# Kernel tuning notes

Hardware: AMD Instinct MI355X
Metric: run time of the kernel (lower is better)

## Reference

```python
import jax, jax.numpy as jnp
import numpy as np
from jax import lax

VOCAB, EMBED, HIDDEN, LAYERS = 32000, 256, 384, 6
B, S = 16, 512
SCALE = 0.05  # keep tanh out of saturation

def setup_inputs() -> dict:
    key = jax.random.key(0)
    ks = jax.random.split(key, 10)
    return {
        "x": jax.random.randint(ks[0], (B, S), 0, VOCAB),
        "emb": jax.random.normal(ks[1], (VOCAB, EMBED), jnp.float32) * SCALE,
        "W_ih0": jax.random.normal(ks[2], (HIDDEN, EMBED), jnp.float32) * SCALE,
        "W_ih": jax.random.normal(ks[3], (LAYERS - 1, HIDDEN, HIDDEN), jnp.float32) * SCALE,
        "W_hh": jax.random.normal(ks[4], (LAYERS, HIDDEN, HIDDEN), jnp.float32) * SCALE,
        "b_ih": jax.random.normal(ks[5], (LAYERS, HIDDEN), jnp.float32) * SCALE,
        "b_hh": jax.random.normal(ks[6], (LAYERS, HIDDEN), jnp.float32) * SCALE,
        "W_out": jax.random.normal(ks[7], (VOCAB, HIDDEN), jnp.float32) * SCALE,
        "b_out": jax.random.normal(ks[8], (VOCAB,), jnp.float32) * SCALE,
    }

def _rnn_layer(seq, Wi, Wh, bi, bh):
    # seq: [S, B, in_dim]; Elman: h_t = tanh(x_t Wi^T + bi + h_{t-1} Wh^T + bh)
    pre = jnp.einsum('sbi,hi->sbh', seq, Wi) + bi  # batched input projection
    h0 = jnp.zeros((seq.shape[1], Wh.shape[0]), seq.dtype)
    def step(h, p):
        h = jnp.tanh(p + h @ Wh.T + bh)
        return h, h
    _, out = lax.scan(step, h0, pre)
    return out  # [S, B, H]

def reference(x, emb, W_ih0, W_ih, W_hh, b_ih, b_hh, W_out, b_out):
    seq = jnp.swapaxes(emb[x], 0, 1)  # [S, B, E]
    for l in range(LAYERS):
        Wi = W_ih0 if l == 0 else W_ih[l - 1]
        seq = _rnn_layer(seq, Wi, W_hh[l], b_ih[l], b_hh[l])
        # inter-layer dropout: identity in eval mode
    out = jnp.swapaxes(seq, 0, 1)  # [B, S, H]
    return out @ W_out.T + b_out  # [B, S, V]
```

## Files before the change

kernel.cpp:

```cpp
#include <hip/hip_runtime.h>

typedef _Float16 f16;
typedef _Float16 f16x8 __attribute__((ext_vector_type(8)));
typedef _Float16 f16x4 __attribute__((ext_vector_type(4)));
typedef float f32x4 __attribute__((ext_vector_type(4)));

#define MFMA16(a, b, c) __builtin_amdgcn_mfma_f32_16x16x32_f16(a, b, c, 0, 0, 0)

#define CH 8
#define NCH 64
#define SLOT_F (CH * 24 * 64 * 4)

__device__ __forceinline__ float fast_tanh(float x) {
    float e = __builtin_amdgcn_exp2f(x * 2.885390081777927f);
    return 1.0f - 2.0f * __builtin_amdgcn_rcpf(e + 1.0f);
}

__device__ __forceinline__ void lds_barrier() {
    asm volatile("s_waitcnt lgkmcnt(0)" ::: "memory");
    __builtin_amdgcn_s_barrier();
    __builtin_amdgcn_sched_barrier(0);
}

__device__ __forceinline__ void wait_flag(const int* f, int target) {
    if (threadIdx.x == 0) {
        while (__hip_atomic_load(f, __ATOMIC_ACQUIRE, __HIP_MEMORY_SCOPE_AGENT) < target) {
            __builtin_amdgcn_s_sleep(1);
        }
    }
    __syncthreads();
}
__device__ __forceinline__ void set_flag(int* f, int val) {
    __syncthreads();
    if (threadIdx.x == 0)
        __hip_atomic_store(f, val, __ATOMIC_RELEASE, __HIP_MEMORY_SCOPE_AGENT);
}

__global__ void cvt_kernel(const float* __restrict__ src, f16* __restrict__ dst, const int n4) {
    const int i = blockIdx.x * blockDim.x + threadIdx.x;
    if (i < n4) {
        const float4 v = ((const float4*)src)[i];
        f16x4 o = { (f16)v.x, (f16)v.y, (f16)v.z, (f16)v.w };
        *(f16x4*)(dst + (size_t)i * 4) = o;
    }
}

__global__ void bias_combine_kernel(const float* __restrict__ b_ih, const float* __restrict__ b_hh,
                                    float* __restrict__ bias_c) {
    const int i = blockIdx.x * blockDim.x + threadIdx.x;
    if (i < 6 * 384) bias_c[i] = b_ih[i] + b_hh[i];
}

__global__ void embed_kernel(const int* __restrict__ x, const float* __restrict__ emb,
                             f16* __restrict__ seq0) {
    const int token = blockIdx.x;
    const int s = token >> 4, b = token & 15;
    const int idx = x[b * 512 + s];
    const float4 v = ((const float4*)(emb + (size_t)idx * 256))[threadIdx.x];
    f16x4 o = { (f16)v.x, (f16)v.y, (f16)v.z, (f16)v.w };
    *(f16x4*)(seq0 + (size_t)token * 256 + threadIdx.x * 4) = o;
}

template<int NK>
__device__ __forceinline__ void a_role(const f16* __restrict__ in_seq,
                                       const f16* __restrict__ Wi,
                                       const float* __restrict__ bias,
                                       float* __restrict__ preL,
                                       const int* flag_in, int* flag_pre, const int* flag_seq,
                                       const int L) {
    const int tid = threadIdx.x, lane = tid & 63, w = tid >> 6;
    const int lr = lane & 15, lq = lane >> 4;
    const int KIN = NK * 32;

    f16x8 WiF[6][NK];
#pragma unroll
    for (int i = 0; i < 6; ++i) {
        const f16* wrow = Wi + (size_t)((w * 6 + i) * 16 + lr) * KIN + lq * 8;
#pragma unroll
        for (int kk = 0; kk < NK; ++kk) WiF[i][kk] = *(const f16x8*)(wrow + kk * 32);
    }
    float bv[6];
#pragma unroll
    for (int i = 0; i < 6; ++i) bv[i] = bias[(w * 6 + i) * 16 + lr];

    for (int c = 0; c < NCH; ++c) {
        if (L > 0) wait_flag(flag_in, c + 1);
        if (c >= 4) wait_flag(flag_seq, c - 3);

        float* slot = preL + (size_t)(c & 3) * SLOT_F;
#pragma unroll
        for (int g = 0; g < 2; ++g) {
            f32x4 acc[4][6];
#pragma unroll
            for (int s = 0; s < 4; ++s)
#pragma unroll
                for (int i = 0; i < 6; ++i) acc[s][i] = (f32x4){ bv[i], bv[i], bv[i], bv[i] };

            const int t0 = c * CH + g * 4;
#pragma unroll
            for (int kk = 0; kk < NK; ++kk) {
                f16x8 a[4];
#pragma unroll
                for (int s = 0; s < 4; ++s)
                    a[s] = *(const f16x8*)(in_seq + (size_t)((t0 + s) * 16 + lr) * KIN + kk * 32 + lq * 8);
#pragma unroll
                for (int s = 0; s < 4; ++s)
#pragma unroll
                    for (int i = 0; i < 6; ++i) acc[s][i] = MFMA16(a[s], WiF[i][kk], acc[s][i]);
            }
#pragma unroll
            for (int s = 0; s < 4; ++s)
#pragma unroll
                for (int i = 0; i < 6; ++i)
                    *(f32x4*)(slot + ((size_t)((g * 4 + s) * 24 + w * 6 + i) * 64 + lane) * 4) = acc[s][i];
        }
        set_flag(flag_pre, c + 1);
    }
}

__device__ __forceinline__ void b_role(const float* __restrict__ preL,
                                       const f16* __restrict__ Wh,
                                       f16* __restrict__ out_seq,
                                       const int* flag_pre, int* flag_seq,
                                       f16 (*hbuf)[16][392]) {
    const int tid = threadIdx.x, lane = tid & 63, w = tid >> 6;
    const int lr = lane & 15, lq = lane >> 4, kb = lq * 8;

    for (int i = tid; i < 2 * 16 * 392; i += 256) (&hbuf[0][0][0])[i] = (f16)0.0f;

    f16x8 WhF[6][12];
#pragma unroll
    for (int i = 0; i < 6; ++i) {
        const f16* wrow = Wh + (size_t)((w * 6 + i) * 16 + lr) * 384 + kb;
#pragma unroll
        for (int kk = 0; kk < 12; ++kk) WhF[i][kk] = *(const f16x8*)(wrow + kk * 32);
    }
    __syncthreads();

    const int crow = tid >> 4;
    const int ccol = (tid & 15) * 8;

    for (int c = 0; c < NCH; ++c) {
        wait_flag(flag_pre, c + 1);
        const float* slot = preL + (size_t)(c & 3) * SLOT_F;

#pragma unroll
        for (int g = 0; g < 2; ++g) {
            f32x4 pre_[4][6];
#pragma unroll
            for (int s = 0; s < 4; ++s)
#pragma unroll
                for (int i = 0; i < 6; ++i)
                    pre_[s][i] = *(const f32x4*)(slot + ((size_t)((g * 4 + s) * 24 + w * 6 + i) * 64 + lane) * 4);

#pragma unroll
            for (int s4 = 0; s4 < 4; ++s4) {
                const int sc = g * 4 + s4;
                const int t = c * CH + sc;
                f32x4 acc[6];
#pragma unroll
                for (int i = 0; i < 6; ++i) acc[i] = (f32x4){ 0.f, 0.f, 0.f, 0.f };

                const f16* hb = &hbuf[sc & 1][0][0] + lr * 392 + kb;
#pragma unroll
                for (int kk = 0; kk < 12; ++kk) {
                    const f16x8 a = *(const f16x8*)(hb + kk * 32);
#pragma unroll
                    for (int i = 0; i < 6; ++i) acc[i] = MFMA16(a, WhF[i][kk], acc[i]);
                }

                f16* hn = &hbuf[(sc + 1) & 1][0][0];
#pragma unroll
                for (int i = 0; i < 6; ++i) {
                    const int n = (w * 6 + i) * 16 + lr;
#pragma unroll
                    for (int r = 0; r < 4; ++r) {
                        const float v = acc[i][r] + pre_[s4][i][r];
                        hn[(lq * 4 + r) * 392 + n] = (f16)fast_tanh(v);
                    }
                }
                lds_barrier();
                const f16* hs = &hbuf[(sc + 1) & 1][0][0] + crow * 392 + ccol;
                f16* og = out_seq + (size_t)(t * 16 + crow) * 384 + ccol;
#pragma unroll
                for (int p = 0; p < 3; ++p)
                    *(f16x8*)(og + p * 128) = *(const f16x8*)(hs + p * 128);
            }
        }
        set_flag(flag_seq, c + 1);
    }
}

__global__ __launch_bounds__(256, 1) void pipeline_kernel(
    const f16* __restrict__ seq0, const f16* __restrict__ Wi0,
    const f16* __restrict__ WiR, const f16* __restrict__ WhAll,
    const float* __restrict__ biasAll, f16* __restrict__ sA, f16* __restrict__ sB,
    float* __restrict__ preRing, int* __restrict__ flags) {
    __shared__ f16 hbuf[2][16][392];
    const int bid = blockIdx.x;
    if (bid < 6) {
        const int L = bid;
        const f16* in_seq = (L == 0) ? seq0 : ((L & 1) ? sA : sB);
        const f16* Wi = (L == 0) ? Wi0 : (WiR + (size_t)(L - 1) * 384 * 384);
        float* preL = preRing + (size_t)L * 4 * SLOT_F;
        if (L == 0)
            a_role<8>(in_seq, Wi, biasAll, preL, nullptr, flags + 8, flags + 0, 0);
        else
            a_role<12>(in_seq, Wi, biasAll + L * 384, preL, flags + (L - 1), flags + 8 + L, flags + L, L);
    } else {
        const int L = bid - 6;
        f16* outb = (L & 1) ? sB : sA;
        b_role(preRing + (size_t)L * 4 * SLOT_F, WhAll + (size_t)L * 384 * 384, outb,
               flags + 8 + L, flags + L, hbuf);
    }
}

__global__ __launch_bounds__(256) void out_proj_kernel(
    const f16* __restrict__ A, const f16* __restrict__ Bm,
    const float* __restrict__ bias, float* __restrict__ C) {
    __shared__ f16 As[128][40];
    __shared__ f16 Bs[128][40];
    const int tid = threadIdx.x, lane = tid & 63, w = tid >> 6;
    const int lr = lane & 15, lq = lane >> 4;
    const int bm = blockIdx.x, bn = blockIdx.y;
    const int wm = w >> 1, wn = w & 1;

    f32x4 acc[4][4];
#pragma unroll
    for (int i = 0; i < 4; ++i)
#pragma unroll
        for (int j = 0; j < 4; ++j) acc[i][j] = (f32x4){ 0.f, 0.f, 0.f, 0.f };

    const int sr = tid >> 1, sh = tid & 1;
    const f16* Ag = A + (size_t)(bm * 128 + sr) * 384 + sh * 16;
    const f16* Bg = Bm + (size_t)(bn * 128 + sr) * 384 + sh * 16;

    for (int kt = 0; kt < 12; ++kt) {
        const f16x8 a0 = *(const f16x8*)(Ag + kt * 32);
        const f16x8 a1 = *(const f16x8*)(Ag + kt * 32 + 8);
        const f16x8 b0 = *(const f16x8*)(Bg + kt * 32);
        const f16x8 b1 = *(const f16x8*)(Bg + kt * 32 + 8);
        *(f16x8*)(&As[sr][sh * 16]) = a0;
        *(f16x8*)(&As[sr][sh * 16 + 8]) = a1;
        *(f16x8*)(&Bs[sr][sh * 16]) = b0;
        *(f16x8*)(&Bs[sr][sh * 16 + 8]) = b1;
        __syncthreads();
        f16x8 af[4], bf[4];
#pragma unroll
        for (int mi = 0; mi < 4; ++mi) af[mi] = *(const f16x8*)(&As[wm * 64 + mi * 16 + lr][lq * 8]);
#pragma unroll
        for (int ni = 0; ni < 4; ++ni) bf[ni] = *(const f16x8*)(&Bs[wn * 64 + ni * 16 + lr][lq * 8]);
#pragma unroll
        for (int mi = 0; mi < 4; ++mi)
#pragma unroll
            for (int ni = 0; ni < 4; ++ni) acc[mi][ni] = MFMA16(af[mi], bf[ni], acc[mi][ni]);
        __syncthreads();
    }

    float bv[4];
#pragma unroll
    for (int ni = 0; ni < 4; ++ni) bv[ni] = bias[bn * 128 + wn * 64 + ni * 16 + lr];
#pragma unroll
    for (int mi = 0; mi < 4; ++mi) {
#pragma unroll
        for (int rr = 0; rr < 4; ++rr) {
            const int m = bm * 128 + wm * 64 + mi * 16 + lq * 4 + rr;
            const int s = m >> 4, b = m & 15;
            float* crow = C + (size_t)(b * 512 + s) * 32000;
#pragma unroll
            for (int ni = 0; ni < 4; ++ni) {
                const int n = bn * 128 + wn * 64 + ni * 16 + lr;
                crow[n] = acc[mi][ni][rr] + bv[ni];
            }
        }
    }
}

extern "C" void kernel_launch(void* const* d_in, const int* in_sizes, int n_in,
                              void* d_out, int out_size, void* d_ws, size_t ws_size,
                              hipStream_t stream) {
    const int* x = (const int*)d_in[0];
    const float* emb = (const float*)d_in[1];
    const float* W_ih0 = (const float*)d_in[2];
    const float* W_ih = (const float*)d_in[3];
    const float* W_hh = (const float*)d_in[4];
    const float* b_ih = (const float*)d_in[5];
    const float* b_hh = (const float*)d_in[6];
    const float* W_out = (const float*)d_in[7];
    const float* b_out = (const float*)d_in[8];
    float* out = (float*)d_out;

    char* ws = (char*)d_ws;
    f16* Wi0_h = (f16*)(ws + 0);
    f16* Wi_h = (f16*)(ws + 196608);
    f16* Wh_h = (f16*)(ws + 1671168);
    f16* Wout_h = (f16*)(ws + 3440640);
    float* bias_c = (float*)(ws + 28016640);
    f16* seq0 = (f16*)(ws + 28025856);
    f16* sA = (f16*)(ws + 32220160);
    f16* sB = (f16*)(ws + 38511616);
    float* preRing = (float*)(ws + 44803072);
    int* flags = (int*)(ws + 49521664);
    if (ws_size < 49521920u) return;

    hipMemsetAsync(flags, 0, 256, stream);
    cvt_kernel<<<96, 256, 0, stream>>>(W_ih0, Wi0_h, 24576);
    cvt_kernel<<<720, 256, 0, stream>>>(W_ih, Wi_h, 184320);
    cvt_kernel<<<864, 256, 0, stream>>>(W_hh, Wh_h, 221184);
    cvt_kernel<<<12000, 256, 0, stream>>>(W_out, Wout_h, 3072000);
    bias_combine_kernel<<<9, 256, 0, stream>>>(b_ih, b_hh, bias_c);
    embed_kernel<<<8192, 64, 0, stream>>>(x, emb, seq0);

    pipeline_kernel<<<12, 256, 0, stream>>>(seq0, Wi0_h, Wi_h, Wh_h, bias_c,
                                            sA, sB, preRing, flags);

    dim3 g(64, 250);
    out_proj_kernel<<<g, 256, 0, stream>>>(sB, Wout_h, b_out, out);
}
```

Measured before the change: 1.913 ms.

## Add coordinator wavefront for cross-block flags and replace block barriers with LDS counters

Each pipeline block gains a fifth wavefront that polls the global flags and mirrors them into LDS control words. Compute waves now spin on LDS instead of taking __syncthreads around every flag wait or set, and the recurrent step barrier becomes an LDS atomic counter. The A role now works one timestep at a time with cache-bypassing loads and staged vmcnt waits, and the B role reads the pre-activation ring with coherent loads. The output projection gets a swizzled 1-D grid for L2 reuse. The cost is harder-to-verify memory ordering and possible spin contention on LDS.

```diff
diff --git a/kernel.cpp b/kernel.cpp
--- a/kernel.cpp
+++ b/kernel.cpp
@@ -11,29 +11,73 @@
 #define NCH 64
 #define SLOT_F (CH * 24 * 64 * 4)
 
+#define IN_READY 0
+#define CREDIT   1
+#define DONE     2
+#define STEP     3
+
 __device__ __forceinline__ float fast_tanh(float x) {
     float e = __builtin_amdgcn_exp2f(x * 2.885390081777927f);
     return 1.0f - 2.0f * __builtin_amdgcn_rcpf(e + 1.0f);
 }
 
-__device__ __forceinline__ void lds_barrier() {
+__device__ __forceinline__ f16x8 ld_llc(const f16* p) {
+    f16x8 v;
+    asm volatile("global_load_dwordx4 %0, %1, off sc0 sc1" : "=v"(v) : "v"(p) : "memory");
+    return v;
+}
+__device__ __forceinline__ f32x4 ld_llc_f32x4(const float* p) {
+    f32x4 v;
+    asm volatile("global_load_dwordx4 %0, %1, off sc0 sc1" : "=v"(v) : "v"(p) : "memory");
+    return v;
+}
+
+#define VWAIT4(N, x0, x1, x2, x3) \
+    asm volatile("s_waitcnt vmcnt(" #N ")" : "+v"(x0), "+v"(x1), "+v"(x2), "+v"(x3))
+#define VWAITP6(N, p0, p1, p2, p3, p4, p5) \
+    asm volatile("s_waitcnt vmcnt(" #N ")" : "+v"(p0), "+v"(p1), "+v"(p2), "+v"(p3), "+v"(p4), "+v"(p5))
+
+__device__ __forceinline__ int lds_ld(const int* p) {
+    return __hip_atomic_load(p, __ATOMIC_ACQUIRE, __HIP_MEMORY_SCOPE_WORKGROUP);
+}
+__device__ __forceinline__ void lds_st(int* p, int v) {
+    __hip_atomic_store(p, v, __ATOMIC_RELEASE, __HIP_MEMORY_SCOPE_WORKGROUP);
+}
+__device__ __forceinline__ void lds_wait_ge(const int* p, int target) {
+    while (lds_ld(p) < target) {}
+    __builtin_amdgcn_sched_barrier(0);
+}
+__device__ __forceinline__ void step_barrier(int* ctr, int target, int lane) {
     asm volatile("s_waitcnt lgkmcnt(0)" ::: "memory");
-    __builtin_amdgcn_s_barrier();
-    __builtin_amdgcn_sched_barrier(0);
-}
-
-__device__ __forceinline__ void wait_flag(const int* f, int target) {
-    if (threadIdx.x == 0) {
-        while (__hip_atomic_load(f, __ATOMIC_ACQUIRE, __HIP_MEMORY_SCOPE_AGENT) < target) {
+    if (lane == 0)
+        __hip_atomic_fetch_add(ctr, 1, __ATOMIC_ACQ_REL, __HIP_MEMORY_SCOPE_WORKGROUP);
+    lds_wait_ge(ctr, target);
+}
+__device__ __forceinline__ void signal_done(int* ctr, int lane) {
+    asm volatile("s_waitcnt vmcnt(0)" ::: "memory");
+    if (lane == 0)
+        __hip_atomic_fetch_add(ctr, 1, __ATOMIC_ACQ_REL, __HIP_MEMORY_SCOPE_WORKGROUP);
+}
+
+__device__ __forceinline__ void coordinator(const int* flag_in, const int* flag_credit,
+                                            int* flag_out, int* ctl,
+                                            bool hasIn, bool hasCredit) {
+    int inr = 0, cr = 0;
+    for (int c = 0; c < NCH; ++c) {
+        const int need = 4 * (c + 1);
+        while (__hip_atomic_load(&ctl[DONE], __ATOMIC_ACQUIRE, __HIP_MEMORY_SCOPE_WORKGROUP) < need) {
+            if (hasIn) {
+                int v = __hip_atomic_load(flag_in, __ATOMIC_RELAXED, __HIP_MEMORY_SCOPE_AGENT);
+                if (v > inr) { inr = v; lds_st(&ctl[IN_READY], v); }
+            }
+            if (hasCredit) {
+                int v = __hip_atomic_load(flag_credit, __ATOMIC_RELAXED, __HIP_MEMORY_SCOPE_AGENT);
+                if (v > cr) { cr = v; lds_st(&ctl[CREDIT], v); }
+            }
             __builtin_amdgcn_s_sleep(1);
         }
-    }
-    __syncthreads();
-}
-__device__ __forceinline__ void set_flag(int* f, int val) {
-    __syncthreads();
-    if (threadIdx.x == 0)
-        __hip_atomic_store(f, val, __ATOMIC_RELEASE, __HIP_MEMORY_SCOPE_AGENT);
+        __hip_atomic_store(flag_out, c + 1, __ATOMIC_RELEASE, __HIP_MEMORY_SCOPE_AGENT);
+    }
 }
 
 __global__ void cvt_kernel(const float* __restrict__ src, f16* __restrict__ dst, const int n4) {
@@ -62,12 +106,11 @@
 }
 
 template<int NK>
-__device__ __forceinline__ void a_role(const f16* __restrict__ in_seq,
-                                       const f16* __restrict__ Wi,
-                                       const float* __restrict__ bias,
-                                       float* __restrict__ preL,
-                                       const int* flag_in, int* flag_pre, const int* flag_seq,
-                                       const int L) {
+__device__ __forceinline__ void a_compute(const f16* __restrict__ in_seq,
+                                          const f16* __restrict__ Wi,
+                                          const float* __restrict__ bias,
+                                          float* __restrict__ preL,
+                                          int* ctl, const int L) {
     const int tid = threadIdx.x, lane = tid & 63, w = tid >> 6;
     const int lr = lane & 15, lq = lane >> 4;
     const int KIN = NK * 32;
@@ -84,50 +127,64 @@
     for (int i = 0; i < 6; ++i) bv[i] = bias[(w * 6 + i) * 16 + lr];
 
     for (int c = 0; c < NCH; ++c) {
-        if (L > 0) wait_flag(flag_in, c + 1);
-        if (c >= 4) wait_flag(flag_seq, c - 3);
+        if (L > 0) lds_wait_ge(&ctl[IN_READY], c + 1);
+        if (c >= 4) lds_wait_ge(&ctl[CREDIT], c - 3);
 
         float* slot = preL + (size_t)(c & 3) * SLOT_F;
-#pragma unroll
-        for (int g = 0; g < 2; ++g) {
-            f32x4 acc[4][6];
-#pragma unroll
-            for (int s = 0; s < 4; ++s)
-#pragma unroll
-                for (int i = 0; i < 6; ++i) acc[s][i] = (f32x4){ bv[i], bv[i], bv[i], bv[i] };
-
-            const int t0 = c * CH + g * 4;
-#pragma unroll
-            for (int kk = 0; kk < NK; ++kk) {
-                f16x8 a[4];
-#pragma unroll
-                for (int s = 0; s < 4; ++s)
-                    a[s] = *(const f16x8*)(in_seq + (size_t)((t0 + s) * 16 + lr) * KIN + kk * 32 + lq * 8);
-#pragma unroll
-                for (int s = 0; s < 4; ++s)
-#pragma unroll
-                    for (int i = 0; i < 6; ++i) acc[s][i] = MFMA16(a[s], WiF[i][kk], acc[s][i]);
+#pragma unroll 1
+        for (int sc = 0; sc < CH; ++sc) {
+            const int t = c * CH + sc;
+            f32x4 acc[6];
+#pragma unroll
+            for (int i = 0; i < 6; ++i) acc[i] = (f32x4){ bv[i], bv[i], bv[i], bv[i] };
+
+            const f16* ar = in_seq + (size_t)(t * 16 + lr) * KIN + lq * 8;
+            f16x8 a[NK];
+#pragma unroll
+            for (int kk = 0; kk < NK; ++kk) a[kk] = ld_llc(ar + kk * 32);
+            if constexpr (NK == 12) {
+                VWAIT4(8, a[0], a[1], a[2], a[3]);
+#pragma unroll
+                for (int kk = 0; kk < 4; ++kk)
+#pragma unroll
+                    for (int i = 0; i < 6; ++i) acc[i] = MFMA16(a[kk], WiF[i][kk], acc[i]);
+                VWAIT4(4, a[4], a[5], a[6], a[7]);
+#pragma unroll
+                for (int kk = 4; kk < 8; ++kk)
+#pragma unroll
+                    for (int i = 0; i < 6; ++i) acc[i] = MFMA16(a[kk], WiF[i][kk], acc[i]);
+                VWAIT4(0, a[8], a[9], a[10], a[11]);
+#pragma unroll
+                for (int kk = 8; kk < 12; ++kk)
+#pragma unroll
+                    for (int i = 0; i < 6; ++i) acc[i] = MFMA16(a[kk], WiF[i][kk], acc[i]);
+            } else {
+                VWAIT4(4, a[0], a[1], a[2], a[3]);
+#pragma unroll
+                for (int kk = 0; kk < 4; ++kk)
+#pragma unroll
+                    for (int i = 0; i < 6; ++i) acc[i] = MFMA16(a[kk], WiF[i][kk], acc[i]);
+                VWAIT4(0, a[4], a[5], a[6], a[7]);
+#pragma unroll
+                for (int kk = 4; kk < 8; ++kk)
+#pragma unroll
+                    for (int i = 0; i < 6; ++i) acc[i] = MFMA16(a[kk], WiF[i][kk], acc[i]);
             }
 #pragma unroll
-            for (int s = 0; s < 4; ++s)
-#pragma unroll
-                for (int i = 0; i < 6; ++i)
-                    *(f32x4*)(slot + ((size_t)((g * 4 + s) * 24 + w * 6 + i) * 64 + lane) * 4) = acc[s][i];
-        }
-        set_flag(flag_pre, c + 1);
-    }
-}
-
-__device__ __forceinline__ void b_role(const float* __restrict__ preL,
-                                       const f16* __restrict__ Wh,
-                                       f16* __restrict__ out_seq,
-                                       const int* flag_pre, int* flag_seq,
-                                       f16 (*hbuf)[16][392]) {
+            for (int i = 0; i < 6; ++i)
+                *(f32x4*)(slot + ((size_t)(sc * 24 + w * 6 + i) * 64 + lane) * 4) = acc[i];
+        }
+        signal_done(&ctl[DONE], lane);
+    }
+}
+
+__device__ __forceinline__ void b_compute(const float* __restrict__ preL,
+                                          const f16* __restrict__ Wh,
+                                          f16* __restrict__ out_seq,
+                                          int* ctl, f16 (*hbuf)[16][392]) {
     const int tid = threadIdx.x, lane = tid & 63, w = tid >> 6;
     const int lr = lane & 15, lq = lane >> 4, kb = lq * 8;
 
-    for (int i = tid; i < 2 * 16 * 392; i += 256) (&hbuf[0][0][0])[i] = (f16)0.0f;
-
     f16x8 WhF[6][12];
 #pragma unroll
     for (int i = 0; i < 6; ++i) {
@@ -135,23 +192,27 @@
 #pragma unroll
         for (int kk = 0; kk < 12; ++kk) WhF[i][kk] = *(const f16x8*)(wrow + kk * 32);
     }
-    __syncthreads();
 
     const int crow = tid >> 4;
     const int ccol = (tid & 15) * 8;
+    int bt = 0;
 
     for (int c = 0; c < NCH; ++c) {
-        wait_flag(flag_pre, c + 1);
+        lds_wait_ge(&ctl[IN_READY], c + 1);
         const float* slot = preL + (size_t)(c & 3) * SLOT_F;
 
-#pragma unroll
+#pragma unroll 1
         for (int g = 0; g < 2; ++g) {
-            f32x4 pre_[4][6];
+            f32x4 pr[4][6];
 #pragma unroll
             for (int s = 0; s < 4; ++s)
 #pragma unroll
                 for (int i = 0; i < 6; ++i)
-                    pre_[s][i] = *(const f32x4*)(slot + ((size_t)((g * 4 + s) * 24 + w * 6 + i) * 64 + lane) * 4);
+                    pr[s][i] = ld_llc_f32x4(slot + ((size_t)((g * 4 + s) * 24 + w * 6 + i) * 64 + lane) * 4);
+            VWAITP6(0, pr[0][0], pr[0][1], pr[0][2], pr[0][3], pr[0][4], pr[0][5]);
+            VWAITP6(0, pr[1][0], pr[1][1], pr[1][2], pr[1][3], pr[1][4], pr[1][5]);
+            VWAITP6(0, pr[2][0], pr[2][1], pr[2][2], pr[2][3], pr[2][4], pr[2][5]);
+            VWAITP6(0, pr[3][0], pr[3][1], pr[3][2], pr[3][3], pr[3][4], pr[3][5]);
 
 #pragma unroll
             for (int s4 = 0; s4 < 4; ++s4) {
@@ -175,11 +236,12 @@
                     const int n = (w * 6 + i) * 16 + lr;
 #pragma unroll
                     for (int r = 0; r < 4; ++r) {
-                        const float v = acc[i][r] + pre_[s4][i][r];
+                        const float v = acc[i][r] + pr[s4][i][r];
                         hn[(lq * 4 + r) * 392 + n] = (f16)fast_tanh(v);
                     }
                 }
-                lds_barrier();
+                ++bt;
+                step_barrier(&ctl[STEP], 4 * bt, lane);
                 const f16* hs = &hbuf[(sc + 1) & 1][0][0] + crow * 392 + ccol;
                 f16* og = out_seq + (size_t)(t * 16 + crow) * 384 + ccol;
 #pragma unroll
@@ -187,31 +249,51 @@
                     *(f16x8*)(og + p * 128) = *(const f16x8*)(hs + p * 128);
             }
         }
-        set_flag(flag_seq, c + 1);
-    }
-}
-
-__global__ __launch_bounds__(256, 1) void pipeline_kernel(
+        signal_done(&ctl[DONE], lane);
+    }
+}
+
+__global__ __launch_bounds__(320, 1) void pipeline_kernel(
     const f16* __restrict__ seq0, const f16* __restrict__ Wi0,
     const f16* __restrict__ WiR, const f16* __restrict__ WhAll,
     const float* __restrict__ biasAll, f16* __restrict__ sA, f16* __restrict__ sB,
     float* __restrict__ preRing, int* __restrict__ flags) {
+    __shared__ int ctl[8];
     __shared__ f16 hbuf[2][16][392];
     const int bid = blockIdx.x;
-    if (bid < 6) {
-        const int L = bid;
-        const f16* in_seq = (L == 0) ? seq0 : ((L & 1) ? sA : sB);
-        const f16* Wi = (L == 0) ? Wi0 : (WiR + (size_t)(L - 1) * 384 * 384);
+    const bool isA = (bid < 6);
+    const int L = isA ? bid : (bid - 6);
+    const int tid = threadIdx.x;
+    const bool isCompute = (tid < 256);
+
+    if (tid == 0) {
+#pragma unroll
+        for (int i = 0; i < 8; ++i) ctl[i] = 0;
+    }
+    if (!isA && isCompute)
+        for (int i = tid; i < 2 * 16 * 392; i += 256) (&hbuf[0][0][0])[i] = (f16)0.0f;
+    __syncthreads();
+
+    if (isA) {
         float* preL = preRing + (size_t)L * 4 * SLOT_F;
-        if (L == 0)
-            a_role<8>(in_seq, Wi, biasAll, preL, nullptr, flags + 8, flags + 0, 0);
-        else
-            a_role<12>(in_seq, Wi, biasAll + L * 384, preL, flags + (L - 1), flags + 8 + L, flags + L, L);
+        if (isCompute) {
+            const f16* in_seq = (L == 0) ? seq0 : ((L & 1) ? sA : sB);
+            if (L == 0)
+                a_compute<8>(in_seq, Wi0, biasAll, preL, ctl, 0);
+            else
+                a_compute<12>(in_seq, WiR + (size_t)(L - 1) * 384 * 384,
+                              biasAll + L * 384, preL, ctl, L);
+        } else if (tid == 256) {
+            coordinator(flags + (L - 1), flags + L, flags + 8 + L, ctl, L > 0, true);
+        }
     } else {
-        const int L = bid - 6;
-        f16* outb = (L & 1) ? sB : sA;
-        b_role(preRing + (size_t)L * 4 * SLOT_F, WhAll + (size_t)L * 384 * 384, outb,
-               flags + 8 + L, flags + L, hbuf);
+        if (isCompute) {
+            f16* outb = (L & 1) ? sB : sA;
+            b_compute(preRing + (size_t)L * 4 * SLOT_F, WhAll + (size_t)L * 384 * 384,
+                      outb, ctl, hbuf);
+        } else if (tid == 256) {
+            coordinator(flags + 8 + L, nullptr, flags + L, ctl, true, false);
+        }
     }
 }
 
@@ -222,7 +304,10 @@
     __shared__ f16 Bs[128][40];
     const int tid = threadIdx.x, lane = tid & 63, w = tid >> 6;
     const int lr = lane & 15, lq = lane >> 4;
-    const int bm = blockIdx.x, bn = blockIdx.y;
+    const int lin = blockIdx.x;
+    const int swz = (lin & 7) * 2000 + (lin >> 3);
+    const int bn = swz >> 6;
+    const int bm = swz & 63;
     const int wm = w >> 1, wn = w & 1;
 
     f32x4 acc[4][4];
@@ -311,9 +396,8 @@
     bias_combine_kernel<<<9, 256, 0, stream>>>(b_ih, b_hh, bias_c);
     embed_kernel<<<8192, 64, 0, stream>>>(x, emb, seq0);
 
-    pipeline_kernel<<<12, 256, 0, stream>>>(seq0, Wi0_h, Wi_h, Wh_h, bias_c,
+    pipeline_kernel<<<12, 320, 0, stream>>>(seq0, Wi0_h, Wi_h, Wh_h, bias_c,
                                             sA, sB, preRing, flags);
 
-    dim3 g(64, 250);
-    out_proj_kernel<<<g, 256, 0, stream>>>(sB, Wout_h, b_out, out);
-}
+    out_proj_kernel<<<16000, 256, 0, stream>>>(sB, Wout_h, b_out, out);
+}
```

New measurement: 4.581 ms. 2.4x slower.
